# Performance work log

Hardware: AMD Instinct MI355X
Metric: run time of the kernel (lower is better)

## Reference

```python
import jax, jax.numpy as jnp
import numpy as np

THETA = 10000.0
NUM_HEADS = 16


def apply_rope(x, pos, theta):
    # x: [..., s, d_k] with d_k even; pos: [s] (broadcasts over leading dims)
    d_k = x.shape[-1]
    inv_freq = 1.0 / (theta ** (jnp.arange(0, d_k, 2, dtype=x.dtype) / d_k))  # [d_k/2]
    ang = pos.astype(x.dtype)[..., None] * inv_freq  # [s, d_k/2]
    cos, sin = jnp.cos(ang), jnp.sin(ang)
    xr = x.reshape(x.shape[:-1] + (d_k // 2, 2))
    x0, x1 = xr[..., 0], xr[..., 1]
    out0 = x0 * cos - x1 * sin
    out1 = x0 * sin + x1 * cos
    return jnp.stack((out0, out1), axis=-1).reshape(x.shape)


def setup_inputs() -> dict:
    key = jax.random.key(0)
    ks = jax.random.split(key, 5)
    B, S, D = 4, 2048, 1024
    sigma = 2.0 / (D + D) ** 0.5
    return {
        "x": jax.random.normal(ks[0], (B, S, D), dtype=jnp.float32),
        "token_positions": jnp.arange(S, dtype=jnp.int64 if jax.config.jax_enable_x64 else jnp.int32),
        "wq": jax.random.normal(ks[1], (D, D), dtype=jnp.float32) * sigma,
        "wk": jax.random.normal(ks[2], (D, D), dtype=jnp.float32) * sigma,
        "wv": jax.random.normal(ks[3], (D, D), dtype=jnp.float32) * sigma,
        "wo": jax.random.normal(ks[4], (D, D), dtype=jnp.float32) * sigma,
    }


def reference(x, token_positions, wq, wk, wv, wo):
    B, S, D = x.shape
    H = NUM_HEADS
    d_k = D // H

    def proj(w, t):  # weight [out, in], t [..., in]
        return jnp.einsum('oi,bsi->bso', w, t)

    def heads(t):  # [b, s, (h d)] -> [b, h, s, d]
        return t.reshape(B, S, H, d_k).transpose(0, 2, 1, 3)

    Q = heads(proj(wq, x))
    K = heads(proj(wk, x))
    V = heads(proj(wv, x))
    Q = apply_rope(Q, token_positions, THETA)
    K = apply_rope(K, token_positions, THETA)

    scores = jnp.einsum('bhqd,bhkd->bhqk', Q, K) * (d_k ** -0.5)
    causal = jnp.tril(jnp.ones((S, S), dtype=bool))
    scores = jnp.where(causal, scores, -jnp.inf)
    attn = jax.nn.softmax(scores.astype(jnp.float32), axis=-1).astype(scores.dtype)
    out = jnp.einsum('bhqk,bhkd->bhqd', attn, V)
    out = out.transpose(0, 2, 1, 3).reshape(B, S, D)
    return jnp.einsum('oi,bsi->bso', wo, out)
```

## Files before the change

### kernel.cpp

```cpp
#include <hip/hip_runtime.h>
#include <cstdint>
#include <cstddef>

#define Bv 4
#define Sv 2048
#define Hv 16
#define Dv 1024
#define Mv (Bv*Sv)

typedef __attribute__((ext_vector_type(8))) short short8;
typedef __attribute__((ext_vector_type(8))) unsigned short ushort8v;
typedef __attribute__((ext_vector_type(4))) float f32x4;

__device__ inline float bf2f(unsigned short u) {
  union { unsigned int i; float f; } x; x.i = ((unsigned int)u) << 16; return x.f;
}
__device__ inline unsigned short f2bf(float f) {
  union { float f; unsigned int i; } x; x.f = f;
  unsigned int r = x.i + 0x7FFFu + ((x.i >> 16) & 1u);
  return (unsigned short)(r >> 16);
}

typedef __attribute__((address_space(1))) const unsigned short gu16;
typedef __attribute__((address_space(3))) unsigned short lu16;
__device__ inline void gld_lds16(const unsigned short* g, unsigned short* l) {
  __builtin_amdgcn_global_load_lds((gu16*)g, (lu16*)l, 16, 0, 0);
}

__global__ __launch_bounds__(256) void prep_all(
    const float* __restrict__ x, const float* __restrict__ wq,
    const float* __restrict__ wk, const float* __restrict__ wv,
    const float* __restrict__ wo, const int* __restrict__ pos,
    unsigned short* __restrict__ xb, unsigned short* __restrict__ wqkvb,
    unsigned short* __restrict__ wob, float* __restrict__ tab) {
  const int bb = blockIdx.x, tid = threadIdx.x;
  if (bb < 8192) {
    int i = bb * 256 + tid;
    float4 v = reinterpret_cast<const float4*>(x)[i];
    ushort4 o;
    o.x = f2bf(v.x); o.y = f2bf(v.y); o.z = f2bf(v.z); o.w = f2bf(v.w);
    reinterpret_cast<ushort4*>(xb)[i] = o;
  } else if (bb < 11264) {
    int i = (bb - 8192) * 256 + tid;
    int w = i >> 18, off = i & 262143;
    const float* src = (w == 0) ? wq : (w == 1) ? wk : wv;
    float4 v = reinterpret_cast<const float4*>(src)[off];
    ushort4 o;
    o.x = f2bf(v.x); o.y = f2bf(v.y); o.z = f2bf(v.z); o.w = f2bf(v.w);
    reinterpret_cast<ushort4*>(wqkvb)[i] = o;
  } else if (bb < 12288) {
    int i = (bb - 11264) * 256 + tid;
    float4 v = reinterpret_cast<const float4*>(wo)[i];
    ushort4 o;
    o.x = f2bf(v.x); o.y = f2bf(v.y); o.z = f2bf(v.z); o.w = f2bf(v.w);
    reinterpret_cast<ushort4*>(wob)[i] = o;
  } else {
    int idx = (bb - 12288) * 256 + tid;
    int s = idx >> 5, i = idx & 31;
    float p = (float)pos[s];
    float a = p * __builtin_exp2f(-0.41524101186092027f * (float)i);
    tab[(s << 6) + i]      = __builtin_cosf(a);
    tab[(s << 6) + 32 + i] = __builtin_sinf(a);
  }
}

__device__ __forceinline__ void xcd_swizzle(int& bm, int& bn) {
  const int nx = gridDim.x;
  const int nwg = nx * gridDim.y;
  int flat = blockIdx.y * nx + blockIdx.x;
  if ((nwg & 7) == 0) {
    int q = nwg >> 3;
    flat = (flat & 7) * q + (flat >> 3);
  }
  bm = (flat / nx) * 128;
  bn = (flat % nx) * 128;
}

__device__ inline void storeC(float* p, float v) { *p = v; }
__device__ inline void storeC(unsigned short* p, float v) { *p = f2bf(v); }

template <typename CT>
__global__ __launch_bounds__(256) void gemm_bt_128(
    const unsigned short* __restrict__ A,
    const unsigned short* __restrict__ B,
    CT* __restrict__ C,
    int M, int N, int K) {
  __shared__ unsigned short As[128 * 32];
  __shared__ unsigned short Bs[128 * 32];
  const int tid = threadIdx.x;
  const int wave = tid >> 6, lane = tid & 63;
  int bm, bn;
  xcd_swizzle(bm, bn);
  const int wr = (wave >> 1) * 64, wc = (wave & 1) * 64;

  f32x4 acc[4][4] = {};

  const int c0 = wave * 2, c1 = c0 + 1;
  const int sr0 = c0 * 16 + (lane >> 2);
  const int sr1 = c1 * 16 + (lane >> 2);
  const int scol = (lane & 3) * 8;

  const unsigned short* gA0 = A + (size_t)(bm + sr0) * K + scol;
  const unsigned short* gA1 = A + (size_t)(bm + sr1) * K + scol;
  const unsigned short* gB0 = B + (size_t)(bn + sr0) * K + scol;
  const unsigned short* gB1 = B + (size_t)(bn + sr1) * K + scol;
  unsigned short* lA0 = &As[c0 * 512];
  unsigned short* lA1 = &As[c1 * 512];
  unsigned short* lB0 = &Bs[c0 * 512];
  unsigned short* lB1 = &Bs[c1 * 512];

  const int fr = lane & 15;
  const int fk = (lane >> 4) * 8;

  for (int k0 = 0; k0 < K; k0 += 32) {
    gld_lds16(gA0 + k0, lA0);
    gld_lds16(gA1 + k0, lA1);
    gld_lds16(gB0 + k0, lB0);
    gld_lds16(gB1 + k0, lB1);
    __syncthreads();
    short8 af[4], bfr[4];
#pragma unroll
    for (int m = 0; m < 4; m++)
      af[m] = *reinterpret_cast<const short8*>(&As[(wr + m * 16 + fr) * 32 + fk]);
#pragma unroll
    for (int n = 0; n < 4; n++)
      bfr[n] = *reinterpret_cast<const short8*>(&Bs[(wc + n * 16 + fr) * 32 + fk]);
#pragma unroll
    for (int m = 0; m < 4; m++)
#pragma unroll
      for (int n = 0; n < 4; n++)
        acc[m][n] = __builtin_amdgcn_mfma_f32_16x16x32_bf16(af[m], bfr[n], acc[m][n], 0, 0, 0);
    __syncthreads();
  }

  const int er = (lane >> 4) * 4, ec = lane & 15;
#pragma unroll
  for (int m = 0; m < 4; m++)
#pragma unroll
    for (int n = 0; n < 4; n++)
#pragma unroll
      for (int r = 0; r < 4; r++) {
        int row = bm + wr + m * 16 + er + r;
        int col = bn + wc + n * 16 + ec;
        storeC(&C[(size_t)row * N + col], acc[m][n][r]);
      }
}

__global__ __launch_bounds__(256) void gemm_qkv(
    const unsigned short* __restrict__ A,
    const unsigned short* __restrict__ B,
    unsigned short* __restrict__ Qp,
    unsigned short* __restrict__ Kp,
    unsigned short* __restrict__ Vt,
    const float* __restrict__ tab) {
  const int K = Dv;
  __shared__ unsigned short As[128 * 32];
  __shared__ unsigned short Bs[128 * 32];
  const int tid = threadIdx.x;
  const int wave = tid >> 6, lane = tid & 63;
  int bm, bn;
  xcd_swizzle(bm, bn);
  const int wr = (wave >> 1) * 64, wc = (wave & 1) * 64;

  f32x4 acc[4][4] = {};

  const int c0 = wave * 2, c1 = c0 + 1;
  const int sr0 = c0 * 16 + (lane >> 2);
  const int sr1 = c1 * 16 + (lane >> 2);
  const int scol = (lane & 3) * 8;

  const unsigned short* gA0 = A + (size_t)(bm + sr0) * K + scol;
  const unsigned short* gA1 = A + (size_t)(bm + sr1) * K + scol;
  const unsigned short* gB0 = B + (size_t)(bn + sr0) * K + scol;
  const unsigned short* gB1 = B + (size_t)(bn + sr1) * K + scol;
  unsigned short* lA0 = &As[c0 * 512];
  unsigned short* lA1 = &As[c1 * 512];
  unsigned short* lB0 = &Bs[c0 * 512];
  unsigned short* lB1 = &Bs[c1 * 512];

  const int fr = lane & 15;
  const int fk = (lane >> 4) * 8;

  for (int k0 = 0; k0 < K; k0 += 32) {
    gld_lds16(gA0 + k0, lA0);
    gld_lds16(gA1 + k0, lA1);
    gld_lds16(gB0 + k0, lB0);
    gld_lds16(gB1 + k0, lB1);
    __syncthreads();
    short8 af[4], bfr[4];
#pragma unroll
    for (int m = 0; m < 4; m++)
      af[m] = *reinterpret_cast<const short8*>(&As[(wr + m * 16 + fr) * 32 + fk]);
#pragma unroll
    for (int n = 0; n < 4; n++)
      bfr[n] = *reinterpret_cast<const short8*>(&Bs[(wc + n * 16 + fr) * 32 + fk]);
#pragma unroll
    for (int m = 0; m < 4; m++)
#pragma unroll
      for (int n = 0; n < 4; n++)
        acc[m][n] = __builtin_amdgcn_mfma_f32_16x16x32_bf16(af[m], bfr[n], acc[m][n], 0, 0, 0);
    __syncthreads();
  }

  const int er = (lane >> 4) * 4, ec = lane & 15;
  const int region = bn >> 10;
  if (region < 2) {
    unsigned short* T = (region == 0) ? Qp : Kp;
#pragma unroll
    for (int m = 0; m < 4; m++)
#pragma unroll
      for (int n = 0; n < 4; n++) {
        const int col = bn + wc + n * 16 + ec;
        const int ccol = col & (Dv - 1);
        const int ii = (ccol & 63) >> 1;
        const bool odd = col & 1;
#pragma unroll
        for (int r = 0; r < 4; r++) {
          int row = bm + wr + m * 16 + er + r;
          int s = row & (Sv - 1);
          float v = acc[m][n][r];
          float pv = __shfl_xor(v, 1);
          float cc = tab[(s << 6) + ii];
          float sn = tab[(s << 6) + 32 + ii];
          float o = odd ? __builtin_fmaf(pv, sn, v * cc)
                        : __builtin_fmaf(v, cc, -(pv * sn));
          T[(size_t)row * Dv + ccol] = f2bf(o);
        }
      }
  } else {
#pragma unroll
    for (int m = 0; m < 4; m++)
#pragma unroll
      for (int n = 0; n < 4; n++) {
        const int dfull = (bn - 2048) + wc + n * 16 + ec;
        const int row0 = bm + wr + m * 16 + er;
        const int bb = row0 >> 11, s = row0 & (Sv - 1);
        const size_t vtrow = ((size_t)bb * 16 + (dfull >> 6)) * 64 + (dfull & 63);
        ushort4 ov;
        ov.x = f2bf(acc[m][n][0]);
        ov.y = f2bf(acc[m][n][1]);
        ov.z = f2bf(acc[m][n][2]);
        ov.w = f2bf(acc[m][n][3]);
        *reinterpret_cast<ushort4*>(Vt + vtrow * Sv + s) = ov;
      }
  }
}

__device__ __forceinline__ void softmax_strip(
    f32x4 (&sacc)[2][4], const bool lastt, const int qrel0,
    float (&mrun2)[2], float (&lrun)[2], f32x4 (&oacc)[2][4],
    unsigned int (&pk)[2][4][2]) {
  const float c1 = 0.18033688011112042f;
#pragma unroll
  for (int qf = 0; qf < 2; ++qf) {
    const int qrel = qrel0 + qf * 16;
    float pv[4][4];
    float mx = -INFINITY;
#pragma unroll
    for (int kf = 0; kf < 4; ++kf)
#pragma unroll
      for (int r = 0; r < 4; ++r) {
        float s = sacc[qf][kf][r];
        if (lastt) s = (kf * 16 + r > qrel) ? -INFINITY : s;
        pv[kf][r] = s;
        mx = fmaxf(mx, s);
      }
    mx = fmaxf(mx, __shfl_xor(mx, 16));
    mx = fmaxf(mx, __shfl_xor(mx, 32));
    float pm = mx * c1;
    if (__any(pm > mrun2[qf] + 8.0f)) {
      float m2 = fmaxf(mrun2[qf], pm);
      float sfq = __builtin_exp2f(mrun2[qf] - m2);
      lrun[qf] *= sfq;
#pragma unroll
      for (int dc = 0; dc < 4; ++dc)
#pragma unroll
        for (int r = 0; r < 4; ++r) oacc[qf][dc][r] *= sfq;
      mrun2[qf] = m2;
    }
    const float nm = -mrun2[qf];
    float ps = 0.f;
#pragma unroll
    for (int kf = 0; kf < 4; ++kf)
#pragma unroll
      for (int r = 0; r < 4; ++r) {
        float p = __builtin_exp2f(__builtin_fmaf(pv[kf][r], c1, nm));
        ps += p;
        pv[kf][r] = p;
      }
    ps += __shfl_xor(ps, 16);
    ps += __shfl_xor(ps, 32);
    lrun[qf] += ps;
#pragma unroll
    for (int kf = 0; kf < 4; ++kf)
#pragma unroll
      for (int hh = 0; hh < 2; ++hh) {
        unsigned int rr;
        asm("v_cvt_pk_bf16_f32 %0, %1, %2"
            : "=v"(rr) : "v"(pv[kf][2 * hh]), "v"(pv[kf][2 * hh + 1]));
        pk[qf][kf][hh] = rr;
      }
  }
}

__device__ __forceinline__ void pv_strip(
    const short8 (&vfr)[2][4], const unsigned int (&pk)[2][4][2],
    f32x4 (&oacc)[2][4], const int idx0, const int idx1, const bool hi) {
#pragma unroll
  for (int ks = 0; ks < 2; ++ks)
#pragma unroll
    for (int qf = 0; qf < 2; ++qf) {
      int ra = __builtin_amdgcn_ds_bpermute(idx0, (int)pk[qf][2 * ks][0]);
      int rb = __builtin_amdgcn_ds_bpermute(idx0, (int)pk[qf][2 * ks + 1][0]);
      int rc = __builtin_amdgcn_ds_bpermute(idx0, (int)pk[qf][2 * ks][1]);
      int rd = __builtin_amdgcn_ds_bpermute(idx0, (int)pk[qf][2 * ks + 1][1]);
      int re = __builtin_amdgcn_ds_bpermute(idx1, (int)pk[qf][2 * ks][0]);
      int rf = __builtin_amdgcn_ds_bpermute(idx1, (int)pk[qf][2 * ks + 1][0]);
      int rg = __builtin_amdgcn_ds_bpermute(idx1, (int)pk[qf][2 * ks][1]);
      int rh = __builtin_amdgcn_ds_bpermute(idx1, (int)pk[qf][2 * ks + 1][1]);
      union { unsigned int u[4]; short8 v; } pw;
      pw.u[0] = hi ? (unsigned)rb : (unsigned)ra;
      pw.u[1] = hi ? (unsigned)rd : (unsigned)rc;
      pw.u[2] = hi ? (unsigned)rf : (unsigned)re;
      pw.u[3] = hi ? (unsigned)rh : (unsigned)rg;
      __builtin_amdgcn_s_setprio(1);
#pragma unroll
      for (int dc = 0; dc < 4; ++dc)
        oacc[qf][dc] = __builtin_amdgcn_mfma_f32_16x16x32_bf16(vfr[ks][dc], pw.v, oacc[qf][dc], 0, 0, 0);
      __builtin_amdgcn_s_setprio(0);
    }
}

__global__ __launch_bounds__(256, 2) void attn_mfma(
    const unsigned short* __restrict__ Q,
    const unsigned short* __restrict__ K,
    const unsigned short* __restrict__ Vt,
    unsigned short* __restrict__ O) {
  __shared__ __align__(16) unsigned short ldsK[3][4096];
  __shared__ __align__(16) unsigned short ldsV[3][4096];
  const int tid = threadIdx.x;
  const int wave = tid >> 6, lane = tid & 63;
  const int g = lane >> 4, m = lane & 15;
  const int F = blockIdx.x;
  const int q7 = F >> 3;
  const int bh = ((F & 7) << 3) | (q7 & 7);
  const int bi = q7 >> 3;
  const int b = bh >> 4, h = bh & 15;
  const int j = bi * 4 + wave;
  const int sA = j, sB = 63 - j;
  const int qA0 = sA * 32, qB0 = sB * 32;
  const int ntA = (sA >> 1) + 1, ntB = (sB >> 1) + 1;
  const int ntBmax = ((63 - bi * 4) >> 1) + 1;
  const size_t qkbase = ((size_t)b * Sv) * Dv + (size_t)h * 64;
  const size_t vtbase = (size_t)bh * 64 * Sv;
  const f32x4 zf = {0.f, 0.f, 0.f, 0.f};

  int srowS[2], scolS[2];
#pragma unroll
  for (int i = 0; i < 2; ++i) {
    int s = ((i * 4 + wave) << 6) + lane;
    int s2 = s ^ ((s >> 3) & 7);
    srowS[i] = s2 >> 3;
    scolS[i] = (s2 & 7) * 8;
  }

  short8 qA[2][2], qB[2][2];
#pragma unroll
  for (int qf = 0; qf < 2; ++qf)
#pragma unroll
    for (int ks = 0; ks < 2; ++ks) {
      qA[qf][ks] = *reinterpret_cast<const short8*>(
          Q + qkbase + (size_t)(qA0 + qf * 16 + m) * Dv + ks * 32 + g * 8);
      qB[qf][ks] = *reinterpret_cast<const short8*>(
          Q + qkbase + (size_t)(qB0 + qf * 16 + m) * Dv + ks * 32 + g * 8);
    }

  int offL[2][4];
#pragma unroll
  for (int ks = 0; ks < 2; ++ks)
#pragma unroll
    for (int f = 0; f < 4; ++f)
      offL[ks][f] = (f * 16 + m) * 64 + ((((ks << 2) + g) ^ (m & 7)) * 8);

  f32x4 oA[2][4] = {}, oB[2][4] = {};
  float mA[2] = {-INFINITY, -INFINITY}, mB[2] = {-INFINITY, -INFINITY};
  float lA[2] = {0.f, 0.f}, lB[2] = {0.f, 0.f};

  const int idx0 = (((g & 1) << 5) + m) << 2;
  const int idx1 = idx0 + 64;
  const bool hi = (g >= 2);
  int qrelA = qA0 + m - 4 * g;
  int qrelB = qB0 + m - 4 * g;

  auto STAGE = [&](int c, int t) {
    const int kb = t << 6;
#pragma unroll
    for (int i = 0; i < 2; ++i) {
      gld_lds16(K + qkbase + (size_t)(kb + srowS[i]) * Dv + scolS[i],
                &ldsK[c][(i * 4 + wave) * 512]);
      gld_lds16(Vt + vtbase + (size_t)srowS[i] * Sv + kb + scolS[i],
                &ldsV[c][(i * 4 + wave) * 512]);
    }
  };

  STAGE(0, 0);
  STAGE(1, 1);
  int cur = 0, bs = 2;

  for (int t = 0; t < ntBmax; ++t) {
    if (t + 1 < ntBmax) {
      asm volatile("s_waitcnt vmcnt(4)" ::: "memory");
    } else {
      asm volatile("s_waitcnt vmcnt(0)" ::: "memory");
    }
    __builtin_amdgcn_sched_barrier(0);
    __builtin_amdgcn_s_barrier();
    if (t + 2 < ntBmax) STAGE(bs, t + 2);

    if (t < ntB) {
      const bool actA = (t < ntA);
      f32x4 sAacc[2][4], sBacc[2][4];
      short8 kfr[4];
#pragma unroll
      for (int kf = 0; kf < 4; ++kf)
        kfr[kf] = *reinterpret_cast<const short8*>(&ldsK[cur][offL[0][kf]]);
      __builtin_amdgcn_s_setprio(1);
#pragma unroll
      for (int qf = 0; qf < 2; ++qf)
#pragma unroll
        for (int kf = 0; kf < 4; ++kf)
          sBacc[qf][kf] = __builtin_amdgcn_mfma_f32_16x16x32_bf16(kfr[kf], qB[qf][0], zf, 0, 0, 0);
      if (actA)
#pragma unroll
        for (int qf = 0; qf < 2; ++qf)
#pragma unroll
          for (int kf = 0; kf < 4; ++kf)
            sAacc[qf][kf] = __builtin_amdgcn_mfma_f32_16x16x32_bf16(kfr[kf], qA[qf][0], zf, 0, 0, 0);
      __builtin_amdgcn_s_setprio(0);
#pragma unroll
      for (int kf = 0; kf < 4; ++kf)
        kfr[kf] = *reinterpret_cast<const short8*>(&ldsK[cur][offL[1][kf]]);
      __builtin_amdgcn_s_setprio(1);
#pragma unroll
      for (int qf = 0; qf < 2; ++qf)
#pragma unroll
        for (int kf = 0; kf < 4; ++kf)
          sBacc[qf][kf] = __builtin_amdgcn_mfma_f32_16x16x32_bf16(kfr[kf], qB[qf][1], sBacc[qf][kf], 0, 0, 0);
      if (actA)
#pragma unroll
        for (int qf = 0; qf < 2; ++qf)
#pragma unroll
          for (int kf = 0; kf < 4; ++kf)
            sAacc[qf][kf] = __builtin_amdgcn_mfma_f32_16x16x32_bf16(kfr[kf], qA[qf][1], sAacc[qf][kf], 0, 0, 0);
      __builtin_amdgcn_s_setprio(0);

      short8 vfr[2][4];
#pragma unroll
      for (int ks = 0; ks < 2; ++ks)
#pragma unroll
        for (int dc = 0; dc < 4; ++dc)
          vfr[ks][dc] = *reinterpret_cast<const short8*>(&ldsV[cur][offL[ks][dc]]);

      unsigned int pkB[2][4][2], pkA[2][4][2];
      softmax_strip(sBacc, t == ntB - 1, qrelB, mB, lB, oB, pkB);
      if (actA) softmax_strip(sAacc, t == ntA - 1, qrelA, mA, lA, oA, pkA);
      pv_strip(vfr, pkB, oB, idx0, idx1, hi);
      if (actA) pv_strip(vfr, pkA, oA, idx0, idx1, hi);

      qrelA -= 64; qrelB -= 64;
    }

    cur = (cur == 2) ? 0 : cur + 1;
    bs = (bs == 2) ? 0 : bs + 1;
  }

#pragma unroll
  for (int qf = 0; qf < 2; ++qf) {
    float rnA = 1.0f / lA[qf];
    float rnB = 1.0f / lB[qf];
    size_t rowA = (size_t)(qA0 + qf * 16 + m);
    size_t rowB = (size_t)(qB0 + qf * 16 + m);
#pragma unroll
    for (int dc = 0; dc < 4; ++dc) {
      ushort4 ov;
      ov.x = f2bf(oA[qf][dc][0] * rnA);
      ov.y = f2bf(oA[qf][dc][1] * rnA);
      ov.z = f2bf(oA[qf][dc][2] * rnA);
      ov.w = f2bf(oA[qf][dc][3] * rnA);
      *reinterpret_cast<ushort4*>(O + qkbase + rowA * Dv + dc * 16 + 4 * g) = ov;
      ov.x = f2bf(oB[qf][dc][0] * rnB);
      ov.y = f2bf(oB[qf][dc][1] * rnB);
      ov.z = f2bf(oB[qf][dc][2] * rnB);
      ov.w = f2bf(oB[qf][dc][3] * rnB);
      *reinterpret_cast<ushort4*>(O + qkbase + rowB * Dv + dc * 16 + 4 * g) = ov;
    }
  }
}

extern "C" void kernel_launch(void* const* d_in, const int* in_sizes, int n_in,
                              void* d_out, int out_size, void* d_ws, size_t ws_size,
                              hipStream_t stream) {
  const float* x   = (const float*)d_in[0];
  const int*   pos = (const int*)d_in[1];
  const float* wq  = (const float*)d_in[2];
  const float* wk  = (const float*)d_in[3];
  const float* wv  = (const float*)d_in[4];
  const float* wo  = (const float*)d_in[5];
  float* out = (float*)d_out;

  char* w = (char*)d_ws;
  unsigned short* xb    = (unsigned short*)(w);
  unsigned short* wqkvb = (unsigned short*)(w + (16u << 20));
  unsigned short* wob   = (unsigned short*)(w + (22u << 20));
  unsigned short* Qp    = (unsigned short*)(w + (24u << 20));
  unsigned short* Kp    = (unsigned short*)(w + (40u << 20));
  unsigned short* Vt    = (unsigned short*)(w + (56u << 20));
  float*          tab   = (float*)(w + (72u << 20));

  prep_all<<<12544, 256, 0, stream>>>(x, wq, wk, wv, wo, pos, xb, wqkvb, wob, tab);

  gemm_qkv<<<dim3(3 * Dv / 128, Mv / 128), 256, 0, stream>>>(xb, wqkvb, Qp, Kp, Vt, tab);

  attn_mfma<<<512, 256, 0, stream>>>(Qp, Kp, Vt, xb);

  gemm_bt_128<float><<<dim3(Dv / 128, Mv / 128), 256, 0, stream>>>(xb, wob, out, Mv, Dv, Dv);
}
```

Baseline: 215.9 us.

## Widen GEMM K-tile to 64 with XOR-swizzled LDS and template softmax masking

Both projection GEMMs now stage 64-wide K slices instead of 32, so each tile does half as many barrier pairs per K step. The LDS layout is XOR-swizzled on the 8-element chunk index to avoid bank conflicts on the fragment reads. Separately, the causal mask in the attention softmax becomes a template parameter, so the unmasked tiles drop the per-element compare/select. The GEMMs double their LDS footprint, which may reduce occupancy, and the kernels are still single-buffered with no prefetch.

```diff
diff --git a/kernel.cpp b/kernel.cpp
--- a/kernel.cpp
+++ b/kernel.cpp
@@ -85,8 +85,8 @@
     const unsigned short* __restrict__ B,
     CT* __restrict__ C,
     int M, int N, int K) {
-  __shared__ unsigned short As[128 * 32];
-  __shared__ unsigned short Bs[128 * 32];
+  __shared__ unsigned short As[128 * 64];
+  __shared__ unsigned short Bs[128 * 64];
   const int tid = threadIdx.x;
   const int wave = tid >> 6, lane = tid & 63;
   int bm, bn;
@@ -95,41 +95,47 @@
 
   f32x4 acc[4][4] = {};
 
-  const int c0 = wave * 2, c1 = c0 + 1;
-  const int sr0 = c0 * 16 + (lane >> 2);
-  const int sr1 = c1 * 16 + (lane >> 2);
-  const int scol = (lane & 3) * 8;
-
-  const unsigned short* gA0 = A + (size_t)(bm + sr0) * K + scol;
-  const unsigned short* gA1 = A + (size_t)(bm + sr1) * K + scol;
-  const unsigned short* gB0 = B + (size_t)(bn + sr0) * K + scol;
-  const unsigned short* gB1 = B + (size_t)(bn + sr1) * K + scol;
-  unsigned short* lA0 = &As[c0 * 512];
-  unsigned short* lA1 = &As[c1 * 512];
-  unsigned short* lB0 = &Bs[c0 * 512];
-  unsigned short* lB1 = &Bs[c1 * 512];
+  int srow[4], scol[4];
+#pragma unroll
+  for (int i = 0; i < 4; ++i) {
+    int c = i * 4 + wave;
+    srow[i] = c * 8 + (lane >> 3);
+    scol[i] = ((lane & 7) ^ ((lane >> 3) & 7)) * 8;
+  }
 
   const int fr = lane & 15;
-  const int fk = (lane >> 4) * 8;
-
-  for (int k0 = 0; k0 < K; k0 += 32) {
-    gld_lds16(gA0 + k0, lA0);
-    gld_lds16(gA1 + k0, lA1);
-    gld_lds16(gB0 + k0, lB0);
-    gld_lds16(gB1 + k0, lB1);
+  const int g_ = lane >> 4;
+  int offA[2][4], offB[2][4];
+#pragma unroll
+  for (int kh = 0; kh < 2; ++kh)
+#pragma unroll
+    for (int m = 0; m < 4; ++m) {
+      offA[kh][m] = (wr + m * 16 + fr) * 64 + ((((kh << 2) + g_) ^ (fr & 7)) * 8);
+      offB[kh][m] = (wc + m * 16 + fr) * 64 + ((((kh << 2) + g_) ^ (fr & 7)) * 8);
+    }
+
+  for (int k0 = 0; k0 < K; k0 += 64) {
+#pragma unroll
+    for (int i = 0; i < 4; ++i) {
+      gld_lds16(A + (size_t)(bm + srow[i]) * K + k0 + scol[i], &As[(i * 4 + wave) * 512]);
+      gld_lds16(B + (size_t)(bn + srow[i]) * K + k0 + scol[i], &Bs[(i * 4 + wave) * 512]);
+    }
     __syncthreads();
-    short8 af[4], bfr[4];
-#pragma unroll
-    for (int m = 0; m < 4; m++)
-      af[m] = *reinterpret_cast<const short8*>(&As[(wr + m * 16 + fr) * 32 + fk]);
-#pragma unroll
-    for (int n = 0; n < 4; n++)
-      bfr[n] = *reinterpret_cast<const short8*>(&Bs[(wc + n * 16 + fr) * 32 + fk]);
-#pragma unroll
-    for (int m = 0; m < 4; m++)
+#pragma unroll
+    for (int kh = 0; kh < 2; ++kh) {
+      short8 af[4], bfr[4];
+#pragma unroll
+      for (int m = 0; m < 4; m++)
+        af[m] = *reinterpret_cast<const short8*>(&As[offA[kh][m]]);
 #pragma unroll
       for (int n = 0; n < 4; n++)
-        acc[m][n] = __builtin_amdgcn_mfma_f32_16x16x32_bf16(af[m], bfr[n], acc[m][n], 0, 0, 0);
+        bfr[n] = *reinterpret_cast<const short8*>(&Bs[offB[kh][n]]);
+#pragma unroll
+      for (int m = 0; m < 4; m++)
+#pragma unroll
+        for (int n = 0; n < 4; n++)
+          acc[m][n] = __builtin_amdgcn_mfma_f32_16x16x32_bf16(af[m], bfr[n], acc[m][n], 0, 0, 0);
+    }
     __syncthreads();
   }
 
@@ -154,8 +160,8 @@
     unsigned short* __restrict__ Vt,
     const float* __restrict__ tab) {
   const int K = Dv;
-  __shared__ unsigned short As[128 * 32];
-  __shared__ unsigned short Bs[128 * 32];
+  __shared__ unsigned short As[128 * 64];
+  __shared__ unsigned short Bs[128 * 64];
   const int tid = threadIdx.x;
   const int wave = tid >> 6, lane = tid & 63;
   int bm, bn;
@@ -164,41 +170,47 @@
 
   f32x4 acc[4][4] = {};
 
-  const int c0 = wave * 2, c1 = c0 + 1;
-  const int sr0 = c0 * 16 + (lane >> 2);
-  const int sr1 = c1 * 16 + (lane >> 2);
-  const int scol = (lane & 3) * 8;
-
-  const unsigned short* gA0 = A + (size_t)(bm + sr0) * K + scol;
-  const unsigned short* gA1 = A + (size_t)(bm + sr1) * K + scol;
-  const unsigned short* gB0 = B + (size_t)(bn + sr0) * K + scol;
-  const unsigned short* gB1 = B + (size_t)(bn + sr1) * K + scol;
-  unsigned short* lA0 = &As[c0 * 512];
-  unsigned short* lA1 = &As[c1 * 512];
-  unsigned short* lB0 = &Bs[c0 * 512];
-  unsigned short* lB1 = &Bs[c1 * 512];
+  int srow[4], scol[4];
+#pragma unroll
+  for (int i = 0; i < 4; ++i) {
+    int c = i * 4 + wave;
+    srow[i] = c * 8 + (lane >> 3);
+    scol[i] = ((lane & 7) ^ ((lane >> 3) & 7)) * 8;
+  }
 
   const int fr = lane & 15;
-  const int fk = (lane >> 4) * 8;
-
-  for (int k0 = 0; k0 < K; k0 += 32) {
-    gld_lds16(gA0 + k0, lA0);
-    gld_lds16(gA1 + k0, lA1);
-    gld_lds16(gB0 + k0, lB0);
-    gld_lds16(gB1 + k0, lB1);
+  const int g_ = lane >> 4;
+  int offA[2][4], offB[2][4];
+#pragma unroll
+  for (int kh = 0; kh < 2; ++kh)
+#pragma unroll
+    for (int m = 0; m < 4; ++m) {
+      offA[kh][m] = (wr + m * 16 + fr) * 64 + ((((kh << 2) + g_) ^ (fr & 7)) * 8);
+      offB[kh][m] = (wc + m * 16 + fr) * 64 + ((((kh << 2) + g_) ^ (fr & 7)) * 8);
+    }
+
+  for (int k0 = 0; k0 < K; k0 += 64) {
+#pragma unroll
+    for (int i = 0; i < 4; ++i) {
+      gld_lds16(A + (size_t)(bm + srow[i]) * K + k0 + scol[i], &As[(i * 4 + wave) * 512]);
+      gld_lds16(B + (size_t)(bn + srow[i]) * K + k0 + scol[i], &Bs[(i * 4 + wave) * 512]);
+    }
     __syncthreads();
-    short8 af[4], bfr[4];
-#pragma unroll
-    for (int m = 0; m < 4; m++)
-      af[m] = *reinterpret_cast<const short8*>(&As[(wr + m * 16 + fr) * 32 + fk]);
-#pragma unroll
-    for (int n = 0; n < 4; n++)
-      bfr[n] = *reinterpret_cast<const short8*>(&Bs[(wc + n * 16 + fr) * 32 + fk]);
-#pragma unroll
-    for (int m = 0; m < 4; m++)
+#pragma unroll
+    for (int kh = 0; kh < 2; ++kh) {
+      short8 af[4], bfr[4];
+#pragma unroll
+      for (int m = 0; m < 4; m++)
+        af[m] = *reinterpret_cast<const short8*>(&As[offA[kh][m]]);
 #pragma unroll
       for (int n = 0; n < 4; n++)
-        acc[m][n] = __builtin_amdgcn_mfma_f32_16x16x32_bf16(af[m], bfr[n], acc[m][n], 0, 0, 0);
+        bfr[n] = *reinterpret_cast<const short8*>(&Bs[offB[kh][n]]);
+#pragma unroll
+      for (int m = 0; m < 4; m++)
+#pragma unroll
+        for (int n = 0; n < 4; n++)
+          acc[m][n] = __builtin_amdgcn_mfma_f32_16x16x32_bf16(af[m], bfr[n], acc[m][n], 0, 0, 0);
+    }
     __syncthreads();
   }
 
@@ -246,8 +258,9 @@
   }
 }
 
+template <bool MASKED>
 __device__ __forceinline__ void softmax_strip(
-    f32x4 (&sacc)[2][4], const bool lastt, const int qrel0,
+    f32x4 (&sacc)[2][4], const int qrel0,
     float (&mrun2)[2], float (&lrun)[2], f32x4 (&oacc)[2][4],
     unsigned int (&pk)[2][4][2]) {
   const float c1 = 0.18033688011112042f;
@@ -261,7 +274,7 @@
 #pragma unroll
       for (int r = 0; r < 4; ++r) {
         float s = sacc[qf][kf][r];
-        if (lastt) s = (kf * 16 + r > qrel) ? -INFINITY : s;
+        if (MASKED) s = (kf * 16 + r > qrel) ? -INFINITY : s;
         pv[kf][r] = s;
         mx = fmaxf(mx, s);
       }
@@ -462,8 +475,12 @@
           vfr[ks][dc] = *reinterpret_cast<const short8*>(&ldsV[cur][offL[ks][dc]]);
 
       unsigned int pkB[2][4][2], pkA[2][4][2];
-      softmax_strip(sBacc, t == ntB - 1, qrelB, mB, lB, oB, pkB);
-      if (actA) softmax_strip(sAacc, t == ntA - 1, qrelA, mA, lA, oA, pkA);
+      if (t == ntB - 1) softmax_strip<true >(sBacc, qrelB, mB, lB, oB, pkB);
+      else              softmax_strip<false>(sBacc, qrelB, mB, lB, oB, pkB);
+      if (actA) {
+        if (t == ntA - 1) softmax_strip<true >(sAacc, qrelA, mA, lA, oA, pkA);
+        else              softmax_strip<false>(sAacc, qrelA, mA, lA, oA, pkA);
+      }
       pv_strip(vfr, pkB, oB, idx0, idx1, hi);
       if (actA) pv_strip(vfr, pkA, oA, idx0, idx1, hi);
 
```

Measured after the change: 201.7 us. -6.6%, faster.

## Double-buffer GEMM LDS tiles with XOR swizzle and specialize masked softmax

Applied to the files above, without the earlier changes.

Both projection GEMMs (generic and fused QKV) now use two LDS buffers. The next K-tile's global-to-LDS load is issued before the current tile's MFMAs, leaving one barrier per iteration instead of two. The LDS column layout is XOR-swizzled on both write and read to reduce bank conflicts, and MFMA sections are raised in wave priority. In attention, softmax_strip is templated on the causal mask so unmasked tiles skip the per-element compare, at the cost of more code size and doubled LDS per GEMM block.

```diff
diff --git a/kernel.cpp b/kernel.cpp
--- a/kernel.cpp
+++ b/kernel.cpp
@@ -85,8 +85,8 @@
     const unsigned short* __restrict__ B,
     CT* __restrict__ C,
     int M, int N, int K) {
-  __shared__ unsigned short As[128 * 32];
-  __shared__ unsigned short Bs[128 * 32];
+  __shared__ unsigned short As[2][128 * 32];
+  __shared__ unsigned short Bs[2][128 * 32];
   const int tid = threadIdx.x;
   const int wave = tid >> 6, lane = tid & 63;
   int bm, bn;
@@ -96,41 +96,57 @@
   f32x4 acc[4][4] = {};
 
   const int c0 = wave * 2, c1 = c0 + 1;
+  const int scol = ((lane & 3) ^ ((lane >> 3) & 3)) * 8;
   const int sr0 = c0 * 16 + (lane >> 2);
   const int sr1 = c1 * 16 + (lane >> 2);
-  const int scol = (lane & 3) * 8;
 
   const unsigned short* gA0 = A + (size_t)(bm + sr0) * K + scol;
   const unsigned short* gA1 = A + (size_t)(bm + sr1) * K + scol;
   const unsigned short* gB0 = B + (size_t)(bn + sr0) * K + scol;
   const unsigned short* gB1 = B + (size_t)(bn + sr1) * K + scol;
-  unsigned short* lA0 = &As[c0 * 512];
-  unsigned short* lA1 = &As[c1 * 512];
-  unsigned short* lB0 = &Bs[c0 * 512];
-  unsigned short* lB1 = &Bs[c1 * 512];
 
   const int fr = lane & 15;
-  const int fk = (lane >> 4) * 8;
-
-  for (int k0 = 0; k0 < K; k0 += 32) {
-    gld_lds16(gA0 + k0, lA0);
-    gld_lds16(gA1 + k0, lA1);
-    gld_lds16(gB0 + k0, lB0);
-    gld_lds16(gB1 + k0, lB1);
-    __syncthreads();
+  const int g_ = lane >> 4;
+  const int fk = (g_ ^ ((fr >> 1) & 3)) * 8;
+  int offA[4], offB[4];
+#pragma unroll
+  for (int m = 0; m < 4; ++m) {
+    offA[m] = (wr + m * 16 + fr) * 32 + fk;
+    offB[m] = (wc + m * 16 + fr) * 32 + fk;
+  }
+
+  const int nt = K >> 5;
+  gld_lds16(gA0, &As[0][c0 * 512]);
+  gld_lds16(gA1, &As[0][c1 * 512]);
+  gld_lds16(gB0, &Bs[0][c0 * 512]);
+  gld_lds16(gB1, &Bs[0][c1 * 512]);
+  __syncthreads();
+  int cur = 0;
+
+  for (int t = 0; t < nt; ++t) {
+    if (t + 1 < nt) {
+      const int k1 = (t + 1) << 5;
+      gld_lds16(gA0 + k1, &As[cur ^ 1][c0 * 512]);
+      gld_lds16(gA1 + k1, &As[cur ^ 1][c1 * 512]);
+      gld_lds16(gB0 + k1, &Bs[cur ^ 1][c0 * 512]);
+      gld_lds16(gB1 + k1, &Bs[cur ^ 1][c1 * 512]);
+    }
     short8 af[4], bfr[4];
 #pragma unroll
     for (int m = 0; m < 4; m++)
-      af[m] = *reinterpret_cast<const short8*>(&As[(wr + m * 16 + fr) * 32 + fk]);
+      af[m] = *reinterpret_cast<const short8*>(&As[cur][offA[m]]);
 #pragma unroll
     for (int n = 0; n < 4; n++)
-      bfr[n] = *reinterpret_cast<const short8*>(&Bs[(wc + n * 16 + fr) * 32 + fk]);
+      bfr[n] = *reinterpret_cast<const short8*>(&Bs[cur][offB[n]]);
+    __builtin_amdgcn_s_setprio(1);
 #pragma unroll
     for (int m = 0; m < 4; m++)
 #pragma unroll
       for (int n = 0; n < 4; n++)
         acc[m][n] = __builtin_amdgcn_mfma_f32_16x16x32_bf16(af[m], bfr[n], acc[m][n], 0, 0, 0);
+    __builtin_amdgcn_s_setprio(0);
     __syncthreads();
+    cur ^= 1;
   }
 
   const int er = (lane >> 4) * 4, ec = lane & 15;
@@ -154,8 +170,8 @@
     unsigned short* __restrict__ Vt,
     const float* __restrict__ tab) {
   const int K = Dv;
-  __shared__ unsigned short As[128 * 32];
-  __shared__ unsigned short Bs[128 * 32];
+  __shared__ unsigned short As[2][128 * 32];
+  __shared__ unsigned short Bs[2][128 * 32];
   const int tid = threadIdx.x;
   const int wave = tid >> 6, lane = tid & 63;
   int bm, bn;
@@ -165,41 +181,57 @@
   f32x4 acc[4][4] = {};
 
   const int c0 = wave * 2, c1 = c0 + 1;
+  const int scol = ((lane & 3) ^ ((lane >> 3) & 3)) * 8;
   const int sr0 = c0 * 16 + (lane >> 2);
   const int sr1 = c1 * 16 + (lane >> 2);
-  const int scol = (lane & 3) * 8;
 
   const unsigned short* gA0 = A + (size_t)(bm + sr0) * K + scol;
   const unsigned short* gA1 = A + (size_t)(bm + sr1) * K + scol;
   const unsigned short* gB0 = B + (size_t)(bn + sr0) * K + scol;
   const unsigned short* gB1 = B + (size_t)(bn + sr1) * K + scol;
-  unsigned short* lA0 = &As[c0 * 512];
-  unsigned short* lA1 = &As[c1 * 512];
-  unsigned short* lB0 = &Bs[c0 * 512];
-  unsigned short* lB1 = &Bs[c1 * 512];
 
   const int fr = lane & 15;
-  const int fk = (lane >> 4) * 8;
-
-  for (int k0 = 0; k0 < K; k0 += 32) {
-    gld_lds16(gA0 + k0, lA0);
-    gld_lds16(gA1 + k0, lA1);
-    gld_lds16(gB0 + k0, lB0);
-    gld_lds16(gB1 + k0, lB1);
-    __syncthreads();
+  const int g_ = lane >> 4;
+  const int fk = (g_ ^ ((fr >> 1) & 3)) * 8;
+  int offA[4], offB[4];
+#pragma unroll
+  for (int m = 0; m < 4; ++m) {
+    offA[m] = (wr + m * 16 + fr) * 32 + fk;
+    offB[m] = (wc + m * 16 + fr) * 32 + fk;
+  }
+
+  const int nt = K >> 5;
+  gld_lds16(gA0, &As[0][c0 * 512]);
+  gld_lds16(gA1, &As[0][c1 * 512]);
+  gld_lds16(gB0, &Bs[0][c0 * 512]);
+  gld_lds16(gB1, &Bs[0][c1 * 512]);
+  __syncthreads();
+  int cur = 0;
+
+  for (int t = 0; t < nt; ++t) {
+    if (t + 1 < nt) {
+      const int k1 = (t + 1) << 5;
+      gld_lds16(gA0 + k1, &As[cur ^ 1][c0 * 512]);
+      gld_lds16(gA1 + k1, &As[cur ^ 1][c1 * 512]);
+      gld_lds16(gB0 + k1, &Bs[cur ^ 1][c0 * 512]);
+      gld_lds16(gB1 + k1, &Bs[cur ^ 1][c1 * 512]);
+    }
     short8 af[4], bfr[4];
 #pragma unroll
     for (int m = 0; m < 4; m++)
-      af[m] = *reinterpret_cast<const short8*>(&As[(wr + m * 16 + fr) * 32 + fk]);
+      af[m] = *reinterpret_cast<const short8*>(&As[cur][offA[m]]);
 #pragma unroll
     for (int n = 0; n < 4; n++)
-      bfr[n] = *reinterpret_cast<const short8*>(&Bs[(wc + n * 16 + fr) * 32 + fk]);
+      bfr[n] = *reinterpret_cast<const short8*>(&Bs[cur][offB[n]]);
+    __builtin_amdgcn_s_setprio(1);
 #pragma unroll
     for (int m = 0; m < 4; m++)
 #pragma unroll
       for (int n = 0; n < 4; n++)
         acc[m][n] = __builtin_amdgcn_mfma_f32_16x16x32_bf16(af[m], bfr[n], acc[m][n], 0, 0, 0);
+    __builtin_amdgcn_s_setprio(0);
     __syncthreads();
+    cur ^= 1;
   }
 
   const int er = (lane >> 4) * 4, ec = lane & 15;
@@ -246,8 +278,9 @@
   }
 }
 
+template <bool MASKED>
 __device__ __forceinline__ void softmax_strip(
-    f32x4 (&sacc)[2][4], const bool lastt, const int qrel0,
+    f32x4 (&sacc)[2][4], const int qrel0,
     float (&mrun2)[2], float (&lrun)[2], f32x4 (&oacc)[2][4],
     unsigned int (&pk)[2][4][2]) {
   const float c1 = 0.18033688011112042f;
@@ -261,7 +294,7 @@
 #pragma unroll
       for (int r = 0; r < 4; ++r) {
         float s = sacc[qf][kf][r];
-        if (lastt) s = (kf * 16 + r > qrel) ? -INFINITY : s;
+        if (MASKED) s = (kf * 16 + r > qrel) ? -INFINITY : s;
         pv[kf][r] = s;
         mx = fmaxf(mx, s);
       }
@@ -462,8 +495,12 @@
           vfr[ks][dc] = *reinterpret_cast<const short8*>(&ldsV[cur][offL[ks][dc]]);
 
       unsigned int pkB[2][4][2], pkA[2][4][2];
-      softmax_strip(sBacc, t == ntB - 1, qrelB, mB, lB, oB, pkB);
-      if (actA) softmax_strip(sAacc, t == ntA - 1, qrelA, mA, lA, oA, pkA);
+      if (t == ntB - 1) softmax_strip<true >(sBacc, qrelB, mB, lB, oB, pkB);
+      else              softmax_strip<false>(sBacc, qrelB, mB, lB, oB, pkB);
+      if (actA) {
+        if (t == ntA - 1) softmax_strip<true >(sAacc, qrelA, mA, lA, oA, pkA);
+        else              softmax_strip<false>(sAacc, qrelA, mA, lA, oA, pkA);
+      }
       pv_strip(vfr, pkB, oB, idx0, idx1, hi);
       if (actA) pv_strip(vfr, pkA, oA, idx0, idx1, hi);
 
```

New measurement: 213.0 us. No clear change (-1.3%).
